# Kernel tuning notes

Measured on AMD Instinct MI355X. Metric: run time of the kernel, lower is better.

Reference implementation:

```python
import jax, jax.numpy as jnp
import numpy as np

N, E, D_IN, D_H, D_OUT = 50000, 800000, 128, 128, 40
EPS = 1e-5


def setup_inputs() -> dict:
    key = jax.random.key(0)
    ks = jax.random.split(key, 12)
    x = jax.random.normal(ks[0], (N, D_IN), dtype=jnp.float32)
    edge_index = jax.random.randint(ks[1], (2, E), 0, N, dtype=jnp.int32)
    s = 1.0 / np.sqrt(D_H)
    return {
        "x": x,
        "edge_index": edge_index,
        "W1": jax.random.normal(ks[2], (D_IN, D_H), jnp.float32) * s,
        "b1": jnp.zeros((D_H,), jnp.float32),
        "W2": jax.random.normal(ks[3], (D_H, D_H), jnp.float32) * s,
        "b2": jnp.zeros((D_H,), jnp.float32),
        "g1": jnp.ones((D_H,), jnp.float32),
        "be1": jnp.zeros((D_H,), jnp.float32),
        "g2": jnp.ones((D_H,), jnp.float32),
        "be2": jnp.zeros((D_H,), jnp.float32),
        "g3": jnp.ones((D_H,), jnp.float32),
        "be3": jnp.zeros((D_H,), jnp.float32),
        "Wm": jax.random.normal(ks[4], (D_H, D_OUT), jnp.float32) * s,
        "bm": jnp.zeros((D_OUT,), jnp.float32),
    }


def _gcn_conv(x, W, b, src, dst, dinv):
    # GCNConv: x' = D^{-1/2}(A+I)D^{-1/2} (x W) + b
    xw = x @ W                                   # [N, H]
    coef = dinv[src] * dinv[dst]                 # [E]
    agg = jax.ops.segment_sum(xw[src] * coef[:, None], dst, num_segments=x.shape[0])
    agg = agg + xw * (dinv * dinv)[:, None]      # self-loop term
    return agg + b


def _bn(x, g, b):
    # BatchNorm1d in training mode: biased batch statistics over nodes
    m = jnp.mean(x, axis=0)
    v = jnp.var(x, axis=0)
    return g * (x - m) * jax.lax.rsqrt(v + EPS) + b


def reference(x, edge_index, W1, b1, W2, b2, g1, be1, g2, be2, g3, be3, Wm, bm):
    src, dst = edge_index[0], edge_index[1]
    # degree with self-loops (GCN symmetric normalization, computed on dst/col)
    deg = 1.0 + jax.ops.segment_sum(jnp.ones((E,), jnp.float32), dst, num_segments=N)
    dinv = jax.lax.rsqrt(deg)
    h = _gcn_conv(x, W1, b1, src, dst, dinv)
    h = jax.nn.relu(_bn(h, g1, be1))            # dropout is identity in eval
    h = _gcn_conv(h, W2, b2, src, dst, dinv)
    h = jax.nn.relu(_bn(h, g2, be2))
    h = _bn(h, g3, be3)
    h = h @ Wm + bm
    return jax.nn.log_softmax(h, axis=1)
```

## Files before the change

kernel.cpp:

```cpp
#include <hip/hip_runtime.h>
#include <hip/hip_fp16.h>
#include <math.h>

#define BN_EPS 1e-5f
#define CAP 128

typedef __attribute__((ext_vector_type(8))) short short8;
typedef __attribute__((ext_vector_type(4))) float floatx4;

__device__ inline unsigned short f2bf(float f) {
    union { float f; unsigned u; } x; x.f = f;
    unsigned r = x.u + 0x7fff + ((x.u >> 16) & 1);
    return (unsigned short)(r >> 16);
}
__device__ inline float bf2f(unsigned short h) {
    union { float f; unsigned u; } x; x.u = ((unsigned)h) << 16; return x.f;
}

__device__ inline void bn_sc_sh(float sum, float sumsq, float g, float be, float invN,
                                float& sc, float& sh) {
    float mean = sum * invN;
    float var = sumsq * invN - mean * mean;
    sc = g * rsqrtf(var + BN_EPS);
    sh = be - mean * sc;
}

__device__ inline void pack_one(int idx, const float* W1, const float* W2, const float* Wm,
                                unsigned short* p1, unsigned short* p2, unsigned short* pm) {
    const float* W;
    unsigned short* pack;
    int f, l = idx & 63, t, n, stride, ncols;
    if (idx < 2048) {
        W = W1; pack = p1; f = idx >> 6; t = f >> 3; n = (f & 7) * 16 + (l & 15);
        stride = 128; ncols = 128;
    } else if (idx < 4096) {
        W = W2; pack = p2; f = (idx - 2048) >> 6; t = f >> 3; n = (f & 7) * 16 + (l & 15);
        stride = 128; ncols = 128;
    } else {
        W = Wm; pack = pm; f = (idx - 4096) >> 6; t = f / 3; n = (f % 3) * 16 + (l & 15);
        stride = 40; ncols = 40;
    }
    int q = l >> 4;
    unsigned short* pp = pack + f * 1024 + l * 16;
#pragma unroll
    for (int j = 0; j < 8; ++j) {
        int k = t * 32 + q * 8 + j;
        float v = (n < ncols) ? W[k * stride + n] : 0.f;
        unsigned short hi = f2bf(v);
        float lo = v - bf2f(hi);
        pp[j] = hi;
        pp[8 + j] = f2bf(lo);
    }
}

__global__ __launch_bounds__(256) void k_pre(const float* __restrict__ W1,
                                             const float* __restrict__ W2,
                                             const float* __restrict__ Wm,
                                             unsigned short* __restrict__ p1,
                                             unsigned short* __restrict__ p2,
                                             unsigned short* __restrict__ pm,
                                             int4* __restrict__ zdst, int nz4) {
    if (blockIdx.x < 19) {
        int idx = blockIdx.x * 256 + threadIdx.x;
        if (idx < 4864) pack_one(idx, W1, W2, Wm, p1, p2, pm);
        return;
    }
    int i = (blockIdx.x - 19) * 256 + threadIdx.x;
    if (i < nz4) zdst[i] = make_int4(0, 0, 0, 0);
}

__device__ inline void load_row8(const float* arow, int kbase, float av[8]) {
    float4 a0 = *(const float4*)(arow + kbase);
    float4 a1 = *(const float4*)(arow + kbase + 4);
    av[0] = a0.x; av[1] = a0.y; av[2] = a0.z; av[3] = a0.w;
    av[4] = a1.x; av[5] = a1.y; av[6] = a1.z; av[7] = a1.w;
}
__device__ inline void load_row8(const __half* arow, int kbase, float av[8]) {
    float4 raw = *(const float4*)(arow + kbase);
    const __half2* h = (const __half2*)&raw;
#pragma unroll
    for (int i = 0; i < 4; ++i) {
        float2 f = __half22float2(h[i]);
        av[2 * i] = f.x;
        av[2 * i + 1] = f.y;
    }
}

template <typename T, bool FUSE_BN>
__device__ __forceinline__ void gemm_body(int bid, const T* __restrict__ A,
                                          const unsigned short* __restrict__ packW,
                                          const float* __restrict__ sums,
                                          const float* __restrict__ g,
                                          const float* __restrict__ be, float invN,
                                          __half* __restrict__ C16, int M) {
    int lane = threadIdx.x & 63;
    int wv = threadIdx.x >> 6;
    int m0 = (bid * 4 + wv) * 32;
    if (m0 >= M) return;
    int row = lane & 15, quad = lane >> 4;
    bool has2 = (m0 + 16 < M);

    floatx4 acc0[8], acc1[8];
#pragma unroll
    for (int nt = 0; nt < 8; ++nt) {
        acc0[nt] = (floatx4){0.f, 0.f, 0.f, 0.f};
        acc1[nt] = (floatx4){0.f, 0.f, 0.f, 0.f};
    }

    const T* arow0 = A + (size_t)(m0 + row) * 128;
    const T* arow1 = A + (size_t)((has2 ? m0 + 16 : m0) + row) * 128;
#pragma unroll
    for (int t = 0; t < 4; ++t) {
        int kbase = t * 32 + quad * 8;
        float av0[8], av1[8];
        load_row8(arow0, kbase, av0);
        load_row8(arow1, kbase, av1);
        if (FUSE_BN) {
#pragma unroll
            for (int j = 0; j < 8; ++j) {
                int c = kbase + j;
                float sc, sh;
                bn_sc_sh(sums[c], sums[128 + c], g[c], be[c], invN, sc, sh);
                av0[j] = fmaxf(av0[j] * sc + sh, 0.f);
                av1[j] = fmaxf(av1[j] * sc + sh, 0.f);
            }
        }
        short8 ah0, al0, ah1, al1;
#pragma unroll
        for (int j = 0; j < 8; ++j) {
            unsigned short hi0 = f2bf(av0[j]);
            ah0[j] = (short)hi0;
            al0[j] = (short)f2bf(av0[j] - bf2f(hi0));
            unsigned short hi1 = f2bf(av1[j]);
            ah1[j] = (short)hi1;
            al1[j] = (short)f2bf(av1[j] - bf2f(hi1));
        }
        const unsigned short* wp = packW + (size_t)(t * 8) * 1024 + lane * 16;
#pragma unroll
        for (int nt = 0; nt < 8; ++nt) {
            short8 wh = *(const short8*)wp;
            short8 wl = *(const short8*)(wp + 8);
            wp += 1024;
            acc0[nt] = __builtin_amdgcn_mfma_f32_16x16x32_bf16(ah0, wh, acc0[nt], 0, 0, 0);
            acc0[nt] = __builtin_amdgcn_mfma_f32_16x16x32_bf16(al0, wh, acc0[nt], 0, 0, 0);
            acc0[nt] = __builtin_amdgcn_mfma_f32_16x16x32_bf16(ah0, wl, acc0[nt], 0, 0, 0);
            acc1[nt] = __builtin_amdgcn_mfma_f32_16x16x32_bf16(ah1, wh, acc1[nt], 0, 0, 0);
            acc1[nt] = __builtin_amdgcn_mfma_f32_16x16x32_bf16(al1, wh, acc1[nt], 0, 0, 0);
            acc1[nt] = __builtin_amdgcn_mfma_f32_16x16x32_bf16(ah1, wl, acc1[nt], 0, 0, 0);
        }
    }

#pragma unroll
    for (int nt = 0; nt < 8; ++nt) {
#pragma unroll
        for (int r = 0; r < 4; ++r) {
            C16[(size_t)(m0 + quad * 4 + r) * 128 + nt * 16 + row] =
                __float2half_rn(acc0[nt][r]);
        }
    }
    if (has2) {
#pragma unroll
        for (int nt = 0; nt < 8; ++nt) {
#pragma unroll
            for (int r = 0; r < 4; ++r) {
                C16[(size_t)(m0 + 16 + quad * 4 + r) * 128 + nt * 16 + row] =
                    __float2half_rn(acc1[nt][r]);
            }
        }
    }
}

__device__ __forceinline__ void fill_body(int b, const int* __restrict__ src,
                                          const int* __restrict__ dst, int E,
                                          int* __restrict__ fillc,
                                          unsigned short* __restrict__ col16, int nfill) {
    int g = b & 7;
    int rank = b >> 3;
    int stride = (nfill >> 3) * 256;
    for (int e = rank * 256 + threadIdx.x; e < E; e += stride) {
        int d = dst[e];
        if ((d & 7) != g) continue;
        int r = atomicAdd(&fillc[d], 1);
        if (r < CAP) col16[(size_t)d * CAP + r] = (unsigned short)src[e];
    }
}

__global__ __launch_bounds__(256) void k_fill_gemm1(const float* __restrict__ x,
                                                    const unsigned short* __restrict__ packW1,
                                                    __half* __restrict__ y16, int M, int ngemm,
                                                    const int* __restrict__ src,
                                                    const int* __restrict__ dst, int E,
                                                    int* __restrict__ fillc,
                                                    unsigned short* __restrict__ col16,
                                                    int nfill) {
    if ((int)blockIdx.x < ngemm) {
        gemm_body<float, false>(blockIdx.x, x, packW1, nullptr, nullptr, nullptr, 0.f, y16, M);
        return;
    }
    fill_body((int)blockIdx.x - ngemm, src, dst, E, fillc, col16, nfill);
}

template <typename T, bool FUSE_BN>
__global__ __launch_bounds__(256) void k_gemm(const T* __restrict__ A,
                                              const unsigned short* __restrict__ packW,
                                              const float* __restrict__ sums,
                                              const float* __restrict__ g,
                                              const float* __restrict__ be, float invN,
                                              __half* __restrict__ C16, int M) {
    gemm_body<T, FUSE_BN>(blockIdx.x, A, packW, sums, g, be, invN, C16, M);
}

__global__ __launch_bounds__(256) void k_gather(const __half2* __restrict__ y16,
                                                const int* __restrict__ fillc,
                                                const unsigned short* __restrict__ col16,
                                                const float* __restrict__ bias,
                                                __half2* __restrict__ out, int N) {
    int wv = threadIdx.x >> 6;
    int lane = threadIdx.x & 63;
    int n = blockIdx.x * 4 + wv;
    if (n >= N) return;
    int degraw = fillc[n];
    float dn = rsqrtf(1.f + (float)degraw);
    float2 self = __half22float2(y16[(size_t)n * 64 + lane]);
    float2 acc;
    acc.x = dn * self.x;
    acc.y = dn * self.y;
    int deg = min(degraw, CAP);
    const unsigned short* cb = col16 + (size_t)n * CAP;
    for (int jb = 0; jb < deg; jb += 64) {
        int cnt = min(64, deg - jb);
        int idx = (lane < cnt) ? (int)cb[jb + lane] : 0;
        float dv = (lane < cnt) ? rsqrtf(1.f + (float)fillc[idx]) : 0.f;
        int jj = 0;
        for (; jj + 8 <= cnt; jj += 8) {
            int s0 = __shfl(idx, jj + 0, 64);
            int s1 = __shfl(idx, jj + 1, 64);
            int s2 = __shfl(idx, jj + 2, 64);
            int s3 = __shfl(idx, jj + 3, 64);
            int s4 = __shfl(idx, jj + 4, 64);
            int s5 = __shfl(idx, jj + 5, 64);
            int s6 = __shfl(idx, jj + 6, 64);
            int s7 = __shfl(idx, jj + 7, 64);
            float w0 = __shfl(dv, jj + 0, 64);
            float w1 = __shfl(dv, jj + 1, 64);
            float w2 = __shfl(dv, jj + 2, 64);
            float w3 = __shfl(dv, jj + 3, 64);
            float w4 = __shfl(dv, jj + 4, 64);
            float w5 = __shfl(dv, jj + 5, 64);
            float w6 = __shfl(dv, jj + 6, 64);
            float w7 = __shfl(dv, jj + 7, 64);
            float2 r0 = __half22float2(y16[(size_t)s0 * 64 + lane]);
            float2 r1 = __half22float2(y16[(size_t)s1 * 64 + lane]);
            float2 r2 = __half22float2(y16[(size_t)s2 * 64 + lane]);
            float2 r3 = __half22float2(y16[(size_t)s3 * 64 + lane]);
            float2 r4 = __half22float2(y16[(size_t)s4 * 64 + lane]);
            float2 r5 = __half22float2(y16[(size_t)s5 * 64 + lane]);
            float2 r6 = __half22float2(y16[(size_t)s6 * 64 + lane]);
            float2 r7 = __half22float2(y16[(size_t)s7 * 64 + lane]);
            acc.x += w0 * r0.x + w1 * r1.x + w2 * r2.x + w3 * r3.x +
                     w4 * r4.x + w5 * r5.x + w6 * r6.x + w7 * r7.x;
            acc.y += w0 * r0.y + w1 * r1.y + w2 * r2.y + w3 * r3.y +
                     w4 * r4.y + w5 * r5.y + w6 * r6.y + w7 * r7.y;
        }
        for (; jj < cnt; ++jj) {
            int s = __shfl(idx, jj, 64);
            float w = __shfl(dv, jj, 64);
            float2 r = __half22float2(y16[(size_t)s * 64 + lane]);
            acc.x += w * r.x;
            acc.y += w * r.y;
        }
    }
    float2 b = *(const float2*)&bias[lane << 1];
    float2 o;
    o.x = dn * acc.x + b.x;
    o.y = dn * acc.y + b.y;
    out[(size_t)n * 64 + lane] = __float22half2_rn(o);
}

template <bool TRANSFORM>
__global__ __launch_bounds__(256) void k_stats(const __half2* __restrict__ h, int N,
                                               const float* __restrict__ sums2,
                                               const float* __restrict__ g2,
                                               const float* __restrict__ be2, float invN,
                                               float* __restrict__ stats) {
    int cp = threadIdx.x & 63;
    int rg = threadIdx.x >> 6;
    int rbeg = blockIdx.x * 256;
    int rend = min(rbeg + 256, N);
    float scx = 1.f, shx = 0.f, scy = 1.f, shy = 0.f;
    if (TRANSFORM) {
        int c = cp * 2;
        bn_sc_sh(sums2[c], sums2[128 + c], g2[c], be2[c], invN, scx, shx);
        bn_sc_sh(sums2[c + 1], sums2[128 + c + 1], g2[c + 1], be2[c + 1], invN, scy, shy);
    }
    float sx = 0.f, sy = 0.f, s2x = 0.f, s2y = 0.f;
    for (int r = rbeg + rg; r < rend; r += 4) {
        float2 v = __half22float2(h[(size_t)r * 64 + cp]);
        if (TRANSFORM) {
            v.x = fmaxf(v.x * scx + shx, 0.f);
            v.y = fmaxf(v.y * scy + shy, 0.f);
        }
        sx += v.x; sy += v.y;
        s2x += v.x * v.x; s2y += v.y * v.y;
    }
    __shared__ float ls[4][256];
    ls[0][threadIdx.x] = sx;
    ls[1][threadIdx.x] = sy;
    ls[2][threadIdx.x] = s2x;
    ls[3][threadIdx.x] = s2y;
    __syncthreads();
    if (threadIdx.x < 64) {
        int t = threadIdx.x;
        float a0 = ls[0][t] + ls[0][t + 64] + ls[0][t + 128] + ls[0][t + 192];
        float a1 = ls[1][t] + ls[1][t + 64] + ls[1][t + 128] + ls[1][t + 192];
        float a2 = ls[2][t] + ls[2][t + 64] + ls[2][t + 128] + ls[2][t + 192];
        float a3 = ls[3][t] + ls[3][t + 64] + ls[3][t + 128] + ls[3][t + 192];
        atomicAdd(&stats[2 * t], a0);
        atomicAdd(&stats[2 * t + 1], a1);
        atomicAdd(&stats[128 + 2 * t], a2);
        atomicAdd(&stats[128 + 2 * t + 1], a3);
    }
}

__global__ __launch_bounds__(256) void k_final(const __half* __restrict__ h,
                                               const float* __restrict__ sums2,
                                               const float* __restrict__ g2,
                                               const float* __restrict__ be2,
                                               const float* __restrict__ sums3,
                                               const float* __restrict__ g3,
                                               const float* __restrict__ be3, float invN,
                                               const unsigned short* __restrict__ packWm,
                                               const float* __restrict__ bm,
                                               float* __restrict__ out, int N) {
    int lane = threadIdx.x & 63;
    int wv = threadIdx.x >> 6;
    int m0 = (blockIdx.x * 4 + wv) * 16;
    if (m0 >= N) return;
    int row = lane & 15, quad = lane >> 4;

    floatx4 acc[3];
#pragma unroll
    for (int nt = 0; nt < 3; ++nt) acc[nt] = (floatx4){0.f, 0.f, 0.f, 0.f};

    const __half* arow = h + (size_t)(m0 + row) * 128;
#pragma unroll
    for (int t = 0; t < 4; ++t) {
        int kbase = t * 32 + quad * 8;
        float av[8];
        load_row8(arow, kbase, av);
#pragma unroll
        for (int j = 0; j < 8; ++j) {
            int c = kbase + j;
            float sc2, sh2, sc3, sh3;
            bn_sc_sh(sums2[c], sums2[128 + c], g2[c], be2[c], invN, sc2, sh2);
            bn_sc_sh(sums3[c], sums3[128 + c], g3[c], be3[c], invN, sc3, sh3);
            av[j] = fmaxf(av[j] * sc2 + sh2, 0.f) * sc3 + sh3;
        }
        short8 ah, al;
#pragma unroll
        for (int j = 0; j < 8; ++j) {
            unsigned short hi = f2bf(av[j]);
            ah[j] = (short)hi;
            al[j] = (short)f2bf(av[j] - bf2f(hi));
        }
        const unsigned short* wp = packWm + (size_t)(t * 3) * 1024 + lane * 16;
#pragma unroll
        for (int nt = 0; nt < 3; ++nt) {
            short8 wh = *(const short8*)wp;
            short8 wl = *(const short8*)(wp + 8);
            wp += 1024;
            acc[nt] = __builtin_amdgcn_mfma_f32_16x16x32_bf16(ah, wh, acc[nt], 0, 0, 0);
            acc[nt] = __builtin_amdgcn_mfma_f32_16x16x32_bf16(al, wh, acc[nt], 0, 0, 0);
            acc[nt] = __builtin_amdgcn_mfma_f32_16x16x32_bf16(ah, wl, acc[nt], 0, 0, 0);
        }
    }

    float bb[3];
#pragma unroll
    for (int nt = 0; nt < 3; ++nt) {
        int col = nt * 16 + row;
        bb[nt] = (col < 40) ? bm[col] : 0.f;
    }
    bool val2 = (row < 8);

#pragma unroll
    for (int r = 0; r < 4; ++r) {
        int m = m0 + quad * 4 + r;
        float v0 = acc[0][r] + bb[0];
        float v1 = acc[1][r] + bb[1];
        float v2 = acc[2][r] + bb[2];
        float mx = fmaxf(v0, v1);
        if (val2) mx = fmaxf(mx, v2);
#pragma unroll
        for (int off = 1; off <= 8; off <<= 1) mx = fmaxf(mx, __shfl_xor(mx, off, 64));
        float s = expf(v0 - mx) + expf(v1 - mx) + (val2 ? expf(v2 - mx) : 0.f);
#pragma unroll
        for (int off = 1; off <= 8; off <<= 1) s += __shfl_xor(s, off, 64);
        float lse = mx + logf(s);
        if (m < N) {
            out[(size_t)m * 40 + row] = v0 - lse;
            out[(size_t)m * 40 + 16 + row] = v1 - lse;
            if (val2) out[(size_t)m * 40 + 32 + row] = v2 - lse;
        }
    }
}

extern "C" void kernel_launch(void* const* d_in, const int* in_sizes, int n_in,
                              void* d_out, int out_size, void* d_ws, size_t ws_size,
                              hipStream_t stream) {
    const float* x   = (const float*)d_in[0];
    const int*   ei  = (const int*)d_in[1];
    const float* W1  = (const float*)d_in[2];
    const float* b1  = (const float*)d_in[3];
    const float* W2  = (const float*)d_in[4];
    const float* b2  = (const float*)d_in[5];
    const float* g1  = (const float*)d_in[6];
    const float* be1 = (const float*)d_in[7];
    const float* g2  = (const float*)d_in[8];
    const float* be2 = (const float*)d_in[9];
    const float* g3  = (const float*)d_in[10];
    const float* be3 = (const float*)d_in[11];
    const float* Wm  = (const float*)d_in[12];
    const float* bm  = (const float*)d_in[13];
    float* out = (float*)d_out;

    int N = in_sizes[0] / 128;
    int E = in_sizes[1] / 2;
    const int* srcs = ei;
    const int* dsts = ei + E;
    float invN = 1.0f / (float)N;

    char* ws = (char*)d_ws;
    size_t off = 0;
    auto alloc = [&](size_t bytes) -> void* {
        void* p = ws + off;
        off += (bytes + 255) & ~(size_t)255;
        return p;
    };
    size_t fill_rounded = (((size_t)N * 4) + 255) & ~(size_t)255;
    int*   fillc   = (int*)alloc((size_t)N * 4);
    float* statsAll= (float*)alloc(3 * 256 * 4);
    float* stats1  = statsAll;
    float* stats2  = statsAll + 256;
    float* stats3  = statsAll + 512;
    unsigned short* col16 = (unsigned short*)alloc((size_t)N * CAP * 2);
    unsigned short* packW1 = (unsigned short*)alloc(32768 * 2);
    unsigned short* packW2 = (unsigned short*)alloc(32768 * 2);
    unsigned short* packWm = (unsigned short*)alloc(12288 * 2);
    __half* y16 = (__half*)alloc((size_t)N * 128 * 2);
    __half* h16 = (__half*)alloc((size_t)N * 128 * 2);
    (void)ws_size; (void)n_in; (void)out_size;

    int nthb = (N + 255) / 256;
    int gatherb = (N + 3) / 4;
    int gfb = (N + 63) / 64;
    int ngemm = (N + 127) / 128;
    const int NFILL = 1024;

    int nz4 = (int)((fill_rounded + 3 * 256 * 4) / 16);
    int zb = (nz4 + 255) / 256;

    k_pre<<<19 + zb, 256, 0, stream>>>(W1, W2, Wm, packW1, packW2, packWm,
                                       (int4*)fillc, nz4);

    k_fill_gemm1<<<ngemm + NFILL, 256, 0, stream>>>(x, packW1, y16, N, ngemm, srcs, dsts, E,
                                                    fillc, col16, NFILL);

    k_gather<<<gatherb, 256, 0, stream>>>((const __half2*)y16, fillc, col16, b1,
                                          (__half2*)h16, N);
    k_stats<false><<<nthb, 256, 0, stream>>>((const __half2*)h16, N, nullptr, nullptr, nullptr,
                                             invN, stats1);

    k_gemm<__half, true><<<ngemm, 256, 0, stream>>>(h16, packW2, stats1, g1, be1, invN,
                                                    y16, N);
    k_gather<<<gatherb, 256, 0, stream>>>((const __half2*)y16, fillc, col16, b2,
                                          (__half2*)h16, N);
    k_stats<false><<<nthb, 256, 0, stream>>>((const __half2*)h16, N, nullptr, nullptr, nullptr,
                                             invN, stats2);

    k_stats<true><<<nthb, 256, 0, stream>>>((const __half2*)h16, N, stats2, g2, be2, invN,
                                            stats3);
    k_final<<<gfb, 256, 0, stream>>>(h16, stats2, g2, be2, stats3, g3, be3, invN, packWm, bm,
                                     out, N);
}
```

Measured before the change: 320.5 us.

## Shrink GEMM wave tile, prefetch A rows, interleave GEMM and fill blocks

Each wave in the 128-wide GEMM now handles 16 rows instead of 32, which doubles the GEMM block count and lowers register use per wave. All four K-slices of the A row are loaded up front, both in the GEMM and in the final classifier kernel, so the loads overlap with the math. The fused fill/GEMM1 launch now interleaves GEMM and edge-fill blocks in chunks of 8, so the two workloads run concurrently instead of GEMM blocks being dispatched first. In exchange, each packed-weight fragment is reused for half as many rows, which raises weight reads from cache.

```diff
diff --git a/kernel.cpp b/kernel.cpp
--- a/kernel.cpp
+++ b/kernel.cpp
@@ -95,45 +95,38 @@
                                           __half* __restrict__ C16, int M) {
     int lane = threadIdx.x & 63;
     int wv = threadIdx.x >> 6;
-    int m0 = (bid * 4 + wv) * 32;
+    int m0 = (bid * 4 + wv) * 16;
     if (m0 >= M) return;
     int row = lane & 15, quad = lane >> 4;
-    bool has2 = (m0 + 16 < M);
-
-    floatx4 acc0[8], acc1[8];
-#pragma unroll
-    for (int nt = 0; nt < 8; ++nt) {
-        acc0[nt] = (floatx4){0.f, 0.f, 0.f, 0.f};
-        acc1[nt] = (floatx4){0.f, 0.f, 0.f, 0.f};
-    }
-
-    const T* arow0 = A + (size_t)(m0 + row) * 128;
-    const T* arow1 = A + (size_t)((has2 ? m0 + 16 : m0) + row) * 128;
+
+    floatx4 acc[8];
+#pragma unroll
+    for (int nt = 0; nt < 8; ++nt) acc[nt] = (floatx4){0.f, 0.f, 0.f, 0.f};
+
+    const T* arow = A + (size_t)(m0 + row) * 128;
+
+    float av[4][8];
+#pragma unroll
+    for (int t = 0; t < 4; ++t) load_row8(arow, t * 32 + quad * 8, av[t]);
+
 #pragma unroll
     for (int t = 0; t < 4; ++t) {
         int kbase = t * 32 + quad * 8;
-        float av0[8], av1[8];
-        load_row8(arow0, kbase, av0);
-        load_row8(arow1, kbase, av1);
         if (FUSE_BN) {
 #pragma unroll
             for (int j = 0; j < 8; ++j) {
                 int c = kbase + j;
                 float sc, sh;
                 bn_sc_sh(sums[c], sums[128 + c], g[c], be[c], invN, sc, sh);
-                av0[j] = fmaxf(av0[j] * sc + sh, 0.f);
-                av1[j] = fmaxf(av1[j] * sc + sh, 0.f);
+                av[t][j] = fmaxf(av[t][j] * sc + sh, 0.f);
             }
         }
-        short8 ah0, al0, ah1, al1;
+        short8 ah, al;
 #pragma unroll
         for (int j = 0; j < 8; ++j) {
-            unsigned short hi0 = f2bf(av0[j]);
-            ah0[j] = (short)hi0;
-            al0[j] = (short)f2bf(av0[j] - bf2f(hi0));
-            unsigned short hi1 = f2bf(av1[j]);
-            ah1[j] = (short)hi1;
-            al1[j] = (short)f2bf(av1[j] - bf2f(hi1));
+            unsigned short hi = f2bf(av[t][j]);
+            ah[j] = (short)hi;
+            al[j] = (short)f2bf(av[t][j] - bf2f(hi));
         }
         const unsigned short* wp = packW + (size_t)(t * 8) * 1024 + lane * 16;
 #pragma unroll
@@ -141,12 +134,9 @@
             short8 wh = *(const short8*)wp;
             short8 wl = *(const short8*)(wp + 8);
             wp += 1024;
-            acc0[nt] = __builtin_amdgcn_mfma_f32_16x16x32_bf16(ah0, wh, acc0[nt], 0, 0, 0);
-            acc0[nt] = __builtin_amdgcn_mfma_f32_16x16x32_bf16(al0, wh, acc0[nt], 0, 0, 0);
-            acc0[nt] = __builtin_amdgcn_mfma_f32_16x16x32_bf16(ah0, wl, acc0[nt], 0, 0, 0);
-            acc1[nt] = __builtin_amdgcn_mfma_f32_16x16x32_bf16(ah1, wh, acc1[nt], 0, 0, 0);
-            acc1[nt] = __builtin_amdgcn_mfma_f32_16x16x32_bf16(al1, wh, acc1[nt], 0, 0, 0);
-            acc1[nt] = __builtin_amdgcn_mfma_f32_16x16x32_bf16(ah1, wl, acc1[nt], 0, 0, 0);
+            acc[nt] = __builtin_amdgcn_mfma_f32_16x16x32_bf16(ah, wh, acc[nt], 0, 0, 0);
+            acc[nt] = __builtin_amdgcn_mfma_f32_16x16x32_bf16(al, wh, acc[nt], 0, 0, 0);
+            acc[nt] = __builtin_amdgcn_mfma_f32_16x16x32_bf16(ah, wl, acc[nt], 0, 0, 0);
         }
     }
 
@@ -155,17 +145,7 @@
 #pragma unroll
         for (int r = 0; r < 4; ++r) {
             C16[(size_t)(m0 + quad * 4 + r) * 128 + nt * 16 + row] =
-                __float2half_rn(acc0[nt][r]);
-        }
-    }
-    if (has2) {
-#pragma unroll
-        for (int nt = 0; nt < 8; ++nt) {
-#pragma unroll
-            for (int r = 0; r < 4; ++r) {
-                C16[(size_t)(m0 + 16 + quad * 4 + r) * 128 + nt * 16 + row] =
-                    __float2half_rn(acc1[nt][r]);
-            }
+                __float2half_rn(acc[nt][r]);
         }
     }
 }
@@ -193,11 +173,17 @@
                                                     int* __restrict__ fillc,
                                                     unsigned short* __restrict__ col16,
                                                     int nfill) {
-    if ((int)blockIdx.x < ngemm) {
-        gemm_body<float, false>(blockIdx.x, x, packW1, nullptr, nullptr, nullptr, 0.f, y16, M);
+    int bid = (int)blockIdx.x;
+    int chunk = bid >> 4;
+    int pos = bid & 15;
+    if (pos < 8) {
+        int u = chunk * 8 + pos;
+        if (u < ngemm)
+            gemm_body<float, false>(u, x, packW1, nullptr, nullptr, nullptr, 0.f, y16, M);
         return;
     }
-    fill_body((int)blockIdx.x - ngemm, src, dst, E, fillc, col16, nfill);
+    int b = chunk * 8 + (pos - 8);
+    if (b < nfill) fill_body(b, src, dst, E, fillc, col16, nfill);
 }
 
 template <typename T, bool FUSE_BN>
@@ -343,25 +329,28 @@
     for (int nt = 0; nt < 3; ++nt) acc[nt] = (floatx4){0.f, 0.f, 0.f, 0.f};
 
     const __half* arow = h + (size_t)(m0 + row) * 128;
+
+    float av[4][8];
+#pragma unroll
+    for (int t = 0; t < 4; ++t) load_row8(arow, t * 32 + quad * 8, av[t]);
+
 #pragma unroll
     for (int t = 0; t < 4; ++t) {
         int kbase = t * 32 + quad * 8;
-        float av[8];
-        load_row8(arow, kbase, av);
 #pragma unroll
         for (int j = 0; j < 8; ++j) {
             int c = kbase + j;
             float sc2, sh2, sc3, sh3;
             bn_sc_sh(sums2[c], sums2[128 + c], g2[c], be2[c], invN, sc2, sh2);
             bn_sc_sh(sums3[c], sums3[128 + c], g3[c], be3[c], invN, sc3, sh3);
-            av[j] = fmaxf(av[j] * sc2 + sh2, 0.f) * sc3 + sh3;
+            av[t][j] = fmaxf(av[t][j] * sc2 + sh2, 0.f) * sc3 + sh3;
         }
         short8 ah, al;
 #pragma unroll
         for (int j = 0; j < 8; ++j) {
-            unsigned short hi = f2bf(av[j]);
+            unsigned short hi = f2bf(av[t][j]);
             ah[j] = (short)hi;
-            al[j] = (short)f2bf(av[j] - bf2f(hi));
+            al[j] = (short)f2bf(av[t][j] - bf2f(hi));
         }
         const unsigned short* wp = packWm + (size_t)(t * 3) * 1024 + lane * 16;
 #pragma unroll
@@ -454,7 +443,7 @@
     int nthb = (N + 255) / 256;
     int gatherb = (N + 3) / 4;
     int gfb = (N + 63) / 64;
-    int ngemm = (N + 127) / 128;
+    int ngemm = (N + 63) / 64;
     const int NFILL = 1024;
 
     int nz4 = (int)((fill_rounded + 3 * 256 * 4) / 16);
@@ -463,8 +452,9 @@
     k_pre<<<19 + zb, 256, 0, stream>>>(W1, W2, Wm, packW1, packW2, packWm,
                                        (int4*)fillc, nz4);
 
-    k_fill_gemm1<<<ngemm + NFILL, 256, 0, stream>>>(x, packW1, y16, N, ngemm, srcs, dsts, E,
-                                                    fillc, col16, NFILL);
+    int nchunk = 128;
+    k_fill_gemm1<<<nchunk * 16, 256, 0, stream>>>(x, packW1, y16, N, ngemm, srcs, dsts, E,
+                                                  fillc, col16, NFILL);
 
     k_gather<<<gatherb, 256, 0, stream>>>((const __half2*)y16, fillc, col16, b1,
                                           (__half2*)h16, N);
```

Measured after the change: 327.8 us. +2.3%, slower.
